# Optimization experiments

Measured on AMD Instinct MI355X. Metric: run time of the kernel, lower is better.

Reference implementation:

```python
import jax, jax.numpy as jnp
import numpy as np

FORGET_BIAS = 1.0  # TF BasicLSTMCell default

B, T, D, H = 64, 1024, 300, 512


def setup_inputs() -> dict:
    key = jax.random.key(0)
    k1, k2, k3 = jax.random.split(key, 3)
    essays = jax.random.normal(k1, (B, T, D), dtype=jnp.float32)
    # TF BasicLSTMCell: single kernel [D+H, 4H], gate order (i, j, f, o)
    W_lstm = jax.random.normal(k2, (D + H, 4 * H), dtype=jnp.float32) * 0.05
    b_lstm = jnp.zeros((4 * H,), dtype=jnp.float32)
    W_dense = jax.random.normal(k3, (H, 1), dtype=jnp.float32) * 0.05
    b_dense = jnp.zeros((1,), dtype=jnp.float32)
    return {"essays": essays, "W_lstm": W_lstm, "b_lstm": b_lstm,
            "W_dense": W_dense, "b_dense": b_dense}


def _lstm_scan(essays, W_lstm, b_lstm):
    # Precompute input projection for all timesteps: [B,T,4H]
    Wx, Wh = W_lstm[:D], W_lstm[D:]
    x_proj = jnp.einsum('btd,dg->btg', essays, Wx) + b_lstm

    def step(carry, xp):
        c, h = carry
        gates = xp + h @ Wh  # [B,4H]
        i, j, f, o = jnp.split(gates, 4, axis=-1)
        new_c = c * jax.nn.sigmoid(f + FORGET_BIAS) + jax.nn.sigmoid(i) * jnp.tanh(j)
        new_h = jnp.tanh(new_c) * jax.nn.sigmoid(o)
        return (new_c, new_h), new_h

    init = (jnp.zeros((essays.shape[0], H), essays.dtype),
            jnp.zeros((essays.shape[0], H), essays.dtype))
    _, hs = jax.lax.scan(step, init, jnp.swapaxes(x_proj, 0, 1))  # hs: [T,B,H]
    return jnp.swapaxes(hs, 0, 1)  # [B,T,H]


def reference(essays, W_lstm, b_lstm, W_dense, b_dense):
    lstm_out = _lstm_scan(essays, W_lstm, b_lstm)      # [B,T,H]
    mot = jnp.mean(lstm_out, axis=1)                   # mean-over-time pooling [B,H]
    preds = jax.nn.sigmoid(mot @ W_dense + b_dense)    # [B,1]
    return preds.reshape(-1)                           # [B]
```

## Files before the change

### kernel.cpp

```cpp
#include <hip/hip_runtime.h>
#include <hip/hip_bf16.h>
#include <stdint.h>

#define B_   64
#define T_   1024
#define D_   300
#define H_   512
#define G4H  2048
#define KP   320

typedef __attribute__((ext_vector_type(8))) short short8;
typedef __attribute__((ext_vector_type(4))) float f32x4;
typedef unsigned long long ull;

__device__ __forceinline__ unsigned short f2bf(float v) {
    __hip_bfloat16 h = __float2bfloat16(v);
    return *reinterpret_cast<unsigned short*>(&h);
}
__device__ __forceinline__ float bf2f(unsigned u) {
    return __uint_as_float(u << 16);
}
__device__ __forceinline__ float sigm(float x) { return 1.f / (1.f + __expf(-x)); }
__device__ __forceinline__ float tanhfast(float x) {
    float e = __expf(2.f * x);
    return 1.f - 2.f / (e + 1.f);
}

#define ASYNC16(g, l)                                                        \
    __builtin_amdgcn_global_load_lds(                                        \
        (const __attribute__((address_space(1))) void*)(g),                  \
        (__attribute__((address_space(3))) void*)(l), 16, 0, 0)

__global__ void cvt_essays(const float* __restrict__ es, unsigned short* __restrict__ Ab) {
    unsigned i = blockIdx.x * 256u + threadIdx.x;
    unsigned row = i / KP;
    unsigned col = i - row * KP;
    float v = (col < D_) ? es[(size_t)row * D_ + col] : 0.f;
    Ab[i] = f2bf(v);
}

__global__ void cvt_misc(const float* __restrict__ Wl, unsigned short* __restrict__ Bt) {
    unsigned i = blockIdx.x * 256u + threadIdx.x;
    unsigned n = i / KP, k = i - n * KP;
    float v = (k < D_) ? Wl[(size_t)k * G4H + n] : 0.f;
    Bt[i] = f2bf(v);
}

__global__ void cvt_wh(const float* __restrict__ Wl, unsigned short* __restrict__ WhTg) {
    unsigned i = blockIdx.x * 256u + threadIdx.x;
    unsigned gc = i & 2047u, k = i >> 11;
    WhTg[(size_t)gc * 512 + k] = f2bf(Wl[(size_t)(300 + k) * G4H + gc]);
}

__global__ __launch_bounds__(256) void gemm_xp(
    const unsigned short* __restrict__ Ab,
    const unsigned short* __restrict__ Bt,
    const float* __restrict__ bias,
    unsigned short* __restrict__ xpr)
{
    __shared__ __align__(16) unsigned short Al[128 * 32];
    __shared__ __align__(16) unsigned short Bl[128 * 32];
    const int tid = threadIdx.x;
    const int w = tid >> 6, lane = tid & 63;
    const int ln = lane & 15, q = lane >> 4;
    const int bx = blockIdx.x;
    const int m0 = (bx >> 4) * 128;
    const int n0 = (bx & 15) * 128;
    const int wr = w >> 1, wc = w & 1;

    f32x4 acc[4][4];
#pragma unroll
    for (int i = 0; i < 4; i++)
#pragma unroll
        for (int j = 0; j < 4; j++) acc[i][j] = (f32x4){0.f, 0.f, 0.f, 0.f};

    for (int k0 = 0; k0 < KP; k0 += 32) {
#pragma unroll
        for (int it = 0; it < 2; ++it) {
            int s = it * 4 + w;
            int c = s * 64 + lane;
            int r = c >> 2;
            int ko = (c & 3) * 8;
            ASYNC16(Ab + (size_t)(m0 + r) * KP + k0 + ko, &Al[s * 512]);
            ASYNC16(Bt + (size_t)(n0 + r) * KP + k0 + ko, &Bl[s * 512]);
        }
        __syncthreads();
        short8 af[4], bf[4];
#pragma unroll
        for (int mt = 0; mt < 4; ++mt)
            af[mt] = *(const short8*)&Al[(wr * 64 + mt * 16 + ln) * 32 + q * 8];
#pragma unroll
        for (int nt = 0; nt < 4; ++nt)
            bf[nt] = *(const short8*)&Bl[(wc * 64 + nt * 16 + ln) * 32 + q * 8];
#pragma unroll
        for (int mt = 0; mt < 4; ++mt)
#pragma unroll
            for (int nt = 0; nt < 4; ++nt)
                acc[mt][nt] = __builtin_amdgcn_mfma_f32_16x16x32_bf16(af[mt], bf[nt], acc[mt][nt], 0, 0, 0);
        __syncthreads();
    }
#pragma unroll
    for (int mt = 0; mt < 4; ++mt) {
#pragma unroll
        for (int nt = 0; nt < 4; ++nt) {
            int col = n0 + wc * 64 + nt * 16 + ln;
            int gate = col >> 9, r9 = col & 511;
            int slice = r9 >> 4, jj = r9 & 15;
            float bb = bias[col];
#pragma unroll
            for (int r = 0; r < 4; ++r) {
                int row = m0 + wr * 64 + mt * 16 + q * 4 + r;
                int t = row & 1023, bglob = row >> 10;
                int g = bglob >> 4, bloc = bglob & 15;
                size_t idx = ((((size_t)t * 4 + g) * 32 + slice) * 16 + bloc) * 64
                             + gate * 16 + jj;
                xpr[idx] = f2bf(acc[mt][nt][r] + bb);
            }
        }
    }
}

__global__ __launch_bounds__(256, 1) void lstm_rec(
    const unsigned short* __restrict__ WhTg,
    const unsigned short* __restrict__ xpr,
    unsigned* __restrict__ hfp,
    float* __restrict__ hmean)
{
    __shared__ __align__(16) unsigned short WhT[64 * 520];
    __shared__ __align__(16) unsigned short hl[16 * 520];
    __shared__ float gbuf[4][16][17];

    const int tid = threadIdx.x;
    const int bid = blockIdx.x;
    const int g     = bid >> 5;
    const int slice = bid & 31;
    const int j0    = slice * 16;
    const int bg    = g * 16;
    const int wv = tid >> 6, lane = tid & 63, ln = lane & 15, q = lane >> 4;

    for (int ch = tid; ch < 64 * 64; ch += 256) {
        int c = ch >> 6, off = (ch & 63) * 8;
        int gc = (c >> 4) * 512 + j0 + (c & 15);
        *(uint4*)&WhT[c * 520 + off] = *(const uint4*)&WhTg[(size_t)gc * 512 + off];
    }

    const int b = tid >> 4;
    const int j = tid & 15;
    const int rowoff = (bg + b) * 512;

    {
        ull* hl8 = (ull*)hl;
#pragma unroll
        for (int i = 0; i < 16; ++i) {
            int c = tid + (i << 8);
            int row = c >> 8, pair = c & 255;
            hl8[(row * 1040 + pair * 8) >> 3] = 0ull;
        }
    }

    float c_st = 0.f, hsum = 0.f;
    const unsigned short* xblk0 = xpr + ((size_t)g * 32 + slice) * 1024 + b * 64 + j;
    unsigned short xc0 = xblk0[0], xc1 = xblk0[16], xc2 = xblk0[32], xc3 = xblk0[48];
    unsigned short xn0 = xc0, xn1 = xc1, xn2 = xc2, xn3 = xc3;

    for (int t = 0; t < T_; ++t) {
        if (t + 1 < T_) {
            const unsigned short* xr = xblk0 + (size_t)(t + 1) * 131072;
            xn0 = xr[0]; xn1 = xr[16]; xn2 = xr[32]; xn3 = xr[48];
        }
        if (t > 0) {
            const ull* src = (const ull*)(hfp + (size_t)(t & 1) * 32768 + bg * 512);
            const unsigned want = (unsigned)((t >> 1) & 3);
            ull v[16];
#pragma unroll
            for (int i = 0; i < 16; ++i)
                v[i] = __hip_atomic_load(src + tid + (i << 8),
                                         __ATOMIC_RELAXED, __HIP_MEMORY_SCOPE_AGENT);
            while (true) {
                unsigned bad = 0u;
#pragma unroll
                for (int i = 0; i < 16; ++i) {
                    unsigned lo = (unsigned)v[i], hi = (unsigned)(v[i] >> 32);
                    bad |= ((((lo & 3u) ^ want) | ((hi & 3u) ^ want)) != 0u) ? (1u << i) : 0u;
                }
                if (!bad) break;
#pragma unroll
                for (int i = 0; i < 16; ++i)
                    if (bad & (1u << i))
                        v[i] = __hip_atomic_load(src + tid + (i << 8),
                                                 __ATOMIC_RELAXED, __HIP_MEMORY_SCOPE_AGENT);
            }
#pragma unroll
            for (int i = 0; i < 16; ++i) {
                int c = tid + (i << 8);
                int row = c >> 8, pair = c & 255;
                unsigned u = (unsigned)f2bf(__uint_as_float((unsigned)v[i]))
                           | ((unsigned)f2bf(__uint_as_float((unsigned)(v[i] >> 32))) << 16);
                *(unsigned*)((char*)hl + row * 1040 + pair * 4) = u;
            }
        }
        __syncthreads();

        f32x4 acc = (f32x4){0.f, 0.f, 0.f, 0.f};
#pragma unroll
        for (int kk = 0; kk < 16; ++kk) {
            short8 av = *(const short8*)&hl[ln * 520 + kk * 32 + q * 8];
            short8 bv = *(const short8*)&WhT[(wv * 16 + ln) * 520 + kk * 32 + q * 8];
            acc = __builtin_amdgcn_mfma_f32_16x16x32_bf16(av, bv, acc, 0, 0, 0);
        }
#pragma unroll
        for (int r = 0; r < 4; ++r)
            gbuf[wv][q * 4 + r][ln] = acc[r];
        __syncthreads();

        float ai  = gbuf[0][b][j] + bf2f((unsigned)xc0);
        float aj  = gbuf[1][b][j] + bf2f((unsigned)xc1);
        float af_ = gbuf[2][b][j] + bf2f((unsigned)xc2);
        float ao  = gbuf[3][b][j] + bf2f((unsigned)xc3);
        float si = sigm(ai), tj = tanhfast(aj);
        float sf = sigm(af_ + 1.0f), so = sigm(ao);
        c_st = c_st * sf + si * tj;
        float h = tanhfast(c_st) * so;
        hsum += h;
        xc0 = xn0; xc1 = xn1; xc2 = xn2; xc3 = xn3;

        unsigned hb = (__float_as_uint(h) & ~3u) | (unsigned)(((t + 1) >> 1) & 3);
        __hip_atomic_store(hfp + (size_t)((t + 1) & 1) * 32768 + rowoff + j0 + j,
                           hb, __ATOMIC_RELAXED, __HIP_MEMORY_SCOPE_AGENT);
    }
    hmean[(size_t)rowoff + j0 + j] = hsum * (1.f / 1024.f);
}

__global__ void dense_out(const float* __restrict__ hmean, const float* __restrict__ Wd,
                          const float* __restrict__ bd, float* __restrict__ out) {
    int bb = blockIdx.x;
    int lane = threadIdx.x;
    float p = 0.f;
    for (int e = lane; e < H_; e += 64) p += hmean[(size_t)bb * H_ + e] * Wd[e];
#pragma unroll
    for (int off = 32; off; off >>= 1) p += __shfl_down(p, off);
    if (lane == 0) out[bb] = 1.f / (1.f + __expf(-(p + bd[0])));
}

extern "C" void kernel_launch(void* const* d_in, const int* in_sizes, int n_in,
                              void* d_out, int out_size, void* d_ws, size_t ws_size,
                              hipStream_t stream) {
    const float* essays  = (const float*)d_in[0];
    const float* W_lstm  = (const float*)d_in[1];
    const float* b_lstm  = (const float*)d_in[2];
    const float* W_dense = (const float*)d_in[3];
    const float* b_dense = (const float*)d_in[4];
    float* out = (float*)d_out;

    char* ws = (char*)d_ws;
    unsigned short* xp   = (unsigned short*)(ws);
    unsigned short* Ab   = (unsigned short*)(ws + 268435456ull);
    unsigned short* Bt   = (unsigned short*)(ws + 310378496ull);
    unsigned short* WhTg = (unsigned short*)(ws + 311689216ull);
    unsigned*       hfp  = (unsigned*)(ws + 268435456ull);
    float*          hm   = (float*)(ws + 268435456ull + 262144ull);

    hipLaunchKernelGGL(cvt_essays, dim3(81920), dim3(256), 0, stream, essays, Ab);
    hipLaunchKernelGGL(cvt_misc,   dim3(2560),  dim3(256), 0, stream, W_lstm, Bt);
    hipLaunchKernelGGL(cvt_wh,     dim3(4096),  dim3(256), 0, stream, W_lstm, WhTg);
    hipLaunchKernelGGL(gemm_xp,    dim3(8192),  dim3(256), 0, stream, Ab, Bt, b_lstm, xp);
    hipLaunchKernelGGL(lstm_rec,   dim3(128),   dim3(256), 0, stream, WhTg, xp, hfp, hm);
    hipLaunchKernelGGL(dense_out,  dim3(64),    dim3(64),  0, stream, hm, W_dense, b_dense, out);
}
```

Before: 3.607 ms.

## Restructure LSTM recurrence into 16 blocks pipelining four batch groups

The recurrent kernel now runs on 16 blocks, each owning a 32-column slice of hidden units across all four batch groups, instead of 128 blocks each owning one group and one slice. The Wh slice is held in registers rather than shared memory. The four groups are processed in turn, and the polling loads for a later group are issued early so their cross-block latency overlaps the current group's MFMA and gate math. Gate values are exchanged with lane shuffles instead of a shared-memory gather buffer, and the xp layout from the GEMM is changed to match. The trade-off is far fewer CUs doing the serial work, plus high register pressure from the register-resident weights.

Measured after the change: 11.84 ms. 3.28x slower.

```diff
diff --git a/kernel.cpp b/kernel.cpp
--- a/kernel.cpp
+++ b/kernel.cpp
@@ -104,16 +104,20 @@
 #pragma unroll
         for (int nt = 0; nt < 4; ++nt) {
             int col = n0 + wc * 64 + nt * 16 + ln;
-            int gate = col >> 9, r9 = col & 511;
-            int slice = r9 >> 4, jj = r9 & 15;
+            int gate = col >> 9, j9 = col & 511;
+            int sl = j9 >> 5, jl = j9 & 31;
+            int wq  = jl >> 3;
+            int uu  = (jl >> 2) & 1;
+            int kk2 = jl & 3;
             float bb = bias[col];
 #pragma unroll
             for (int r = 0; r < 4; ++r) {
                 int row = m0 + wr * 64 + mt * 16 + q * 4 + r;
                 int t = row & 1023, bglob = row >> 10;
-                int g = bglob >> 4, bloc = bglob & 15;
-                size_t idx = ((((size_t)t * 4 + g) * 32 + slice) * 16 + bloc) * 64
-                             + gate * 16 + jj;
+                int g = bglob >> 4, b = bglob & 15;
+                int tidl = wq * 64 + (b >> 2) * 16 + kk2 * 4 + (b & 3);
+                size_t idx = ((((size_t)t * 4 + g) * 16 + sl) * 256 + tidl) * 8
+                             + uu * 4 + gate;
                 xpr[idx] = f2bf(acc[mt][nt][r] + bb);
             }
         }
@@ -126,109 +130,127 @@
     unsigned* __restrict__ hfp,
     float* __restrict__ hmean)
 {
-    __shared__ __align__(16) unsigned short WhT[64 * 520];
-    __shared__ __align__(16) unsigned short hl[16 * 520];
-    __shared__ float gbuf[4][16][17];
+    __shared__ __align__(16) unsigned short hl[4][16 * 520];
 
     const int tid = threadIdx.x;
-    const int bid = blockIdx.x;
-    const int g     = bid >> 5;
-    const int slice = bid & 31;
-    const int j0    = slice * 16;
-    const int bg    = g * 16;
-    const int wv = tid >> 6, lane = tid & 63, ln = lane & 15, q = lane >> 4;
-
-    for (int ch = tid; ch < 64 * 64; ch += 256) {
-        int c = ch >> 6, off = (ch & 63) * 8;
-        int gc = (c >> 4) * 512 + j0 + (c & 15);
-        *(uint4*)&WhT[c * 520 + off] = *(const uint4*)&WhTg[(size_t)gc * 512 + off];
-    }
-
-    const int b = tid >> 4;
-    const int j = tid & 15;
-    const int rowoff = (bg + b) * 512;
-
-    {
-        ull* hl8 = (ull*)hl;
-#pragma unroll
-        for (int i = 0; i < 16; ++i) {
-            int c = tid + (i << 8);
-            int row = c >> 8, pair = c & 255;
-            hl8[(row * 1040 + pair * 8) >> 3] = 0ull;
-        }
-    }
-
-    float c_st = 0.f, hsum = 0.f;
-    const unsigned short* xblk0 = xpr + ((size_t)g * 32 + slice) * 1024 + b * 64 + j;
-    unsigned short xc0 = xblk0[0], xc1 = xblk0[16], xc2 = xblk0[32], xc3 = xblk0[48];
-    unsigned short xn0 = xc0, xn1 = xc1, xn2 = xc2, xn3 = xc3;
+    const int sl  = blockIdx.x;
+    const int w = tid >> 6, lane = tid & 63, ln = lane & 15, q = lane >> 4;
+    const int m = ln & 3;
+
+    short8 bv[2][16];
+#pragma unroll
+    for (int u = 0; u < 2; ++u) {
+        int gc = (ln & 3) * 512 + 32 * sl + w * 8 + u * 4 + (ln >> 2);
+        const unsigned short* wp = WhTg + (size_t)gc * 512 + q * 8;
+#pragma unroll
+        for (int kk = 0; kk < 16; ++kk)
+            bv[u][kk] = *(const short8*)(wp + kk * 32);
+    }
+    for (int i2 = tid; i2 < 16640; i2 += 256) ((unsigned*)hl)[i2] = 0u;
+    __syncthreads();
+
+    float cst[4][2]  = {{0.f,0.f},{0.f,0.f},{0.f,0.f},{0.f,0.f}};
+    float hsum[4][2] = {{0.f,0.f},{0.f,0.f},{0.f,0.f},{0.f,0.f}};
+    short8 xc[4], xn[4];
+#pragma unroll
+    for (int g = 0; g < 4; ++g)
+        xc[g] = *(const short8*)&xpr[(((size_t)g * 16 + sl) * 256 + tid) * 8];
+
+    ull vE[16], vO[16];
 
     for (int t = 0; t < T_; ++t) {
-        if (t + 1 < T_) {
-            const unsigned short* xr = xblk0 + (size_t)(t + 1) * 131072;
-            xn0 = xr[0]; xn1 = xr[16]; xn2 = xr[32]; xn3 = xr[48];
-        }
-        if (t > 0) {
-            const ull* src = (const ull*)(hfp + (size_t)(t & 1) * 32768 + bg * 512);
-            const unsigned want = (unsigned)((t >> 1) & 3);
-            ull v[16];
-#pragma unroll
-            for (int i = 0; i < 16; ++i)
-                v[i] = __hip_atomic_load(src + tid + (i << 8),
-                                         __ATOMIC_RELAXED, __HIP_MEMORY_SCOPE_AGENT);
-            while (true) {
-                unsigned bad = 0u;
+#pragma unroll
+        for (int p = 0; p < 4; ++p) {
+            const int g = p;
+            ull* v = (p & 1) ? vO : vE;
+            if (t > 0) {
+                const ull* src = (const ull*)(hfp + (size_t)(t & 1) * 32768 + g * 8192);
+                const unsigned want = (unsigned)((t >> 1) & 3);
+                while (true) {
+                    unsigned bad = 0u;
+#pragma unroll
+                    for (int i = 0; i < 16; ++i) {
+                        unsigned lo = (unsigned)v[i], hi = (unsigned)(v[i] >> 32);
+                        bad |= ((((lo & 3u) ^ want) | ((hi & 3u) ^ want)) != 0u) ? (1u << i) : 0u;
+                    }
+                    if (!bad) break;
+#pragma unroll
+                    for (int i = 0; i < 16; ++i)
+                        if (bad & (1u << i))
+                            v[i] = __hip_atomic_load(src + tid + (i << 8),
+                                                     __ATOMIC_RELAXED, __HIP_MEMORY_SCOPE_AGENT);
+                }
 #pragma unroll
                 for (int i = 0; i < 16; ++i) {
-                    unsigned lo = (unsigned)v[i], hi = (unsigned)(v[i] >> 32);
-                    bad |= ((((lo & 3u) ^ want) | ((hi & 3u) ^ want)) != 0u) ? (1u << i) : 0u;
+                    unsigned uu = (unsigned)f2bf(__uint_as_float((unsigned)v[i]))
+                                | ((unsigned)f2bf(__uint_as_float((unsigned)(v[i] >> 32))) << 16);
+                    *(unsigned*)((char*)&hl[g][0] + i * 1040 + tid * 4) = uu;
                 }
-                if (!bad) break;
-#pragma unroll
-                for (int i = 0; i < 16; ++i)
-                    if (bad & (1u << i))
-                        v[i] = __hip_atomic_load(src + tid + (i << 8),
+            }
+            if (t + 1 < T_)
+                xn[g] = *(const short8*)&xpr[((((size_t)(t + 1) * 4 + g) * 16 + sl) * 256 + tid) * 8];
+            __syncthreads();
+
+            f32x4 a0 = (f32x4){0.f,0.f,0.f,0.f}, a1 = (f32x4){0.f,0.f,0.f,0.f};
+            f32x4 b0 = (f32x4){0.f,0.f,0.f,0.f}, b1 = (f32x4){0.f,0.f,0.f,0.f};
+#pragma unroll
+            for (int kk = 0; kk < 8; ++kk) {
+                short8 av = *(const short8*)&hl[g][ln * 520 + kk * 32 + q * 8];
+                a0 = __builtin_amdgcn_mfma_f32_16x16x32_bf16(av, bv[0][kk], a0, 0, 0, 0);
+                a1 = __builtin_amdgcn_mfma_f32_16x16x32_bf16(av, bv[1][kk], a1, 0, 0, 0);
+            }
+#pragma unroll
+            for (int kk = 8; kk < 16; ++kk) {
+                short8 av = *(const short8*)&hl[g][ln * 520 + kk * 32 + q * 8];
+                b0 = __builtin_amdgcn_mfma_f32_16x16x32_bf16(av, bv[0][kk], b0, 0, 0, 0);
+                b1 = __builtin_amdgcn_mfma_f32_16x16x32_bf16(av, bv[1][kk], b1, 0, 0, 0);
+            }
+#pragma unroll
+            for (int u = 0; u < 2; ++u) {
+                f32x4 ca = u ? a1 : a0, cb = u ? b1 : b0;
+                float x0 = ca[0] + cb[0], x1 = ca[1] + cb[1];
+                float x2 = ca[2] + cb[2], x3 = ca[3] + cb[3];
+                float s0 = (m & 1) ? x0 : x1, s1 = (m & 1) ? x2 : x3;
+                s0 = __shfl_xor(s0, 1); s1 = __shfl_xor(s1, 1);
+                if (m & 1) { x0 = s0; x2 = s1; } else { x1 = s0; x3 = s1; }
+                float u0 = (m & 2) ? x0 : x2, u1 = (m & 2) ? x1 : x3;
+                u0 = __shfl_xor(u0, 2); u1 = __shfl_xor(u1, 2);
+                if (m & 2) { x0 = u0; x1 = u1; } else { x2 = u0; x3 = u1; }
+                float ai  = x0 + bf2f((unsigned)(unsigned short)xc[g][u * 4 + 0]);
+                float aj  = x1 + bf2f((unsigned)(unsigned short)xc[g][u * 4 + 1]);
+                float af_ = x2 + bf2f((unsigned)(unsigned short)xc[g][u * 4 + 2]);
+                float ao  = x3 + bf2f((unsigned)(unsigned short)xc[g][u * 4 + 3]);
+                float si = sigm(ai), tj = tanhfast(aj);
+                float sf = sigm(af_ + 1.0f), so = sigm(ao);
+                cst[g][u] = cst[g][u] * sf + si * tj;
+                float h = tanhfast(cst[g][u]) * so;
+                hsum[g][u] += h;
+                unsigned hb = (__float_as_uint(h) & ~3u) | (unsigned)(((t + 1) >> 1) & 3);
+                int b = q * 4 + m, jl = w * 8 + u * 4 + (ln >> 2);
+                __hip_atomic_store(hfp + (size_t)((t + 1) & 1) * 32768 + (g * 16 + b) * 512 + 32 * sl + jl,
+                                   hb, __ATOMIC_RELAXED, __HIP_MEMORY_SCOPE_AGENT);
+            }
+            xc[g] = xn[g];
+            {
+                const int gq = (p + 2) & 3;
+                const int ts = (p < 2) ? t : (t + 1);
+                if (ts >= 1 && ts < T_) {
+                    const ull* src2 = (const ull*)(hfp + (size_t)(ts & 1) * 32768 + gq * 8192);
+#pragma unroll
+                    for (int i = 0; i < 16; ++i)
+                        v[i] = __hip_atomic_load(src2 + tid + (i << 8),
                                                  __ATOMIC_RELAXED, __HIP_MEMORY_SCOPE_AGENT);
-            }
-#pragma unroll
-            for (int i = 0; i < 16; ++i) {
-                int c = tid + (i << 8);
-                int row = c >> 8, pair = c & 255;
-                unsigned u = (unsigned)f2bf(__uint_as_float((unsigned)v[i]))
-                           | ((unsigned)f2bf(__uint_as_float((unsigned)(v[i] >> 32))) << 16);
-                *(unsigned*)((char*)hl + row * 1040 + pair * 4) = u;
-            }
-        }
-        __syncthreads();
-
-        f32x4 acc = (f32x4){0.f, 0.f, 0.f, 0.f};
-#pragma unroll
-        for (int kk = 0; kk < 16; ++kk) {
-            short8 av = *(const short8*)&hl[ln * 520 + kk * 32 + q * 8];
-            short8 bv = *(const short8*)&WhT[(wv * 16 + ln) * 520 + kk * 32 + q * 8];
-            acc = __builtin_amdgcn_mfma_f32_16x16x32_bf16(av, bv, acc, 0, 0, 0);
-        }
-#pragma unroll
-        for (int r = 0; r < 4; ++r)
-            gbuf[wv][q * 4 + r][ln] = acc[r];
-        __syncthreads();
-
-        float ai  = gbuf[0][b][j] + bf2f((unsigned)xc0);
-        float aj  = gbuf[1][b][j] + bf2f((unsigned)xc1);
-        float af_ = gbuf[2][b][j] + bf2f((unsigned)xc2);
-        float ao  = gbuf[3][b][j] + bf2f((unsigned)xc3);
-        float si = sigm(ai), tj = tanhfast(aj);
-        float sf = sigm(af_ + 1.0f), so = sigm(ao);
-        c_st = c_st * sf + si * tj;
-        float h = tanhfast(c_st) * so;
-        hsum += h;
-        xc0 = xn0; xc1 = xn1; xc2 = xn2; xc3 = xn3;
-
-        unsigned hb = (__float_as_uint(h) & ~3u) | (unsigned)(((t + 1) >> 1) & 3);
-        __hip_atomic_store(hfp + (size_t)((t + 1) & 1) * 32768 + rowoff + j0 + j,
-                           hb, __ATOMIC_RELAXED, __HIP_MEMORY_SCOPE_AGENT);
-    }
-    hmean[(size_t)rowoff + j0 + j] = hsum * (1.f / 1024.f);
+                }
+            }
+        }
+    }
+#pragma unroll
+    for (int g = 0; g < 4; ++g)
+#pragma unroll
+        for (int u = 0; u < 2; ++u) {
+            int b = q * 4 + m, jl = w * 8 + u * 4 + (ln >> 2);
+            hmean[(size_t)(g * 16 + b) * 512 + 32 * sl + jl] = hsum[g][u] * (1.f / 1024.f);
+        }
 }
 
 __global__ void dense_out(const float* __restrict__ hmean, const float* __restrict__ Wd,
@@ -264,6 +286,6 @@
     hipLaunchKernelGGL(cvt_misc,   dim3(2560),  dim3(256), 0, stream, W_lstm, Bt);
     hipLaunchKernelGGL(cvt_wh,     dim3(4096),  dim3(256), 0, stream, W_lstm, WhTg);
     hipLaunchKernelGGL(gemm_xp,    dim3(8192),  dim3(256), 0, stream, Ab, Bt, b_lstm, xp);
-    hipLaunchKernelGGL(lstm_rec,   dim3(128),   dim3(256), 0, stream, WhTg, xp, hfp, hm);
+    hipLaunchKernelGGL(lstm_rec,   dim3(16),    dim3(256), 0, stream, WhTg, xp, hfp, hm);
     hipLaunchKernelGGL(dense_out,  dim3(64),    dim3(64),  0, stream, hm, W_dense, b_dense, out);
 }
```
